# Performance work log

Hardware: AMD Instinct MI355X
Metric: run time of the kernel (lower is better)

## Reference

```python
import jax, jax.numpy as jnp
import numpy as np

NUM_CLASSES = 8
SCORE_T = 0.5
IOU_T = 0.5
POSE_HYPS = 10
MAX_DET = 100
B, A = 1, 4096


def _pairwise_iou(bx):
    # bx: (N,4) in (x1,y1,x2,y2); TF-style +1 pixel convention
    x1 = jnp.maximum(bx[:, None, 0], bx[None, :, 0])
    y1 = jnp.maximum(bx[:, None, 1], bx[None, :, 1])
    x2 = jnp.minimum(bx[:, None, 2], bx[None, :, 2])
    y2 = jnp.minimum(bx[:, None, 3], bx[None, :, 3])
    wid = x2 - x1 + 1.0
    hei = y2 - y1 + 1.0
    inter = wid * hei
    area = (bx[:, 2] - bx[:, 0] + 1.0) * (bx[:, 3] - bx[:, 1] + 1.0)
    den = area[:, None] + area[None, :] - inter
    ov = jnp.where(den == 0.0, 0.0, inter / jnp.where(den == 0.0, 1.0, den))  # divide_no_nan
    return jnp.where((wid <= 0.0) | (hei <= 0.0), 0.0, ov)


def _per_class(scores_c, boxes_c, poses_c, conf_c):
    # Fixed-shape re-expression of _filter_detections: instead of compacting the
    # boxes with score > threshold (dynamic shape), keep all N and mask invalid
    # boxes out of the overlap indicator. Relative ordering (which drives the
    # argmax tie-break and the ascending sort) is identical to the compacted
    # subset, so the math matches exactly.
    N = scores_c.shape[0]
    K = POSE_HYPS + 1
    valid = scores_c > SCORE_T
    m = jnp.sum(valid.astype(jnp.int32))  # number of selected boxes
    ov = _pairwise_iou(boxes_c)  # (N,N)
    ind = ((ov > IOU_T) & valid[:, None] & valid[None, :]).astype(jnp.float32)
    # scatter_nd: true_ov[argmax_col(row i), i] = max(row i); column i is unique per update
    max_col = jnp.argmax(ind, axis=1)
    true_ov = jnp.zeros_like(ind).at[max_col, jnp.arange(N)].add(jnp.max(ind, axis=1))
    bc = (1.0 - ov) * true_ov * conf_c[None, :]
    bc = jnp.where(bc == 0.0, 1000.0, bc)  # 1000 = sentinel for 'not a hypothesis'
    # Only the first min(pose_hyps+1, m) ascending-sorted entries per row survive the
    # sequence mask, so take the K smallest instead of a full argsort (same result;
    # top_k of the negation breaks ties by lowest index like a stable ascending sort).
    neg, args = jax.lax.top_k(-bc, K)
    svals = -neg  # (N,K) K smallest per row
    hyp = (jnp.arange(K) < jnp.minimum(K, m)).astype(jnp.float32)
    cmask = jnp.where(svals == 1000.0, 0.0, 1.0) * hyp[None, :]
    denom = jnp.sum(cmask, axis=1)  # (N,)
    safe = jnp.where(denom == 0.0, 1.0, denom)
    poses_avg = jnp.where(denom[:, None] == 0.0, 0.0,
                          jnp.sum(cmask[:, :, None] * poses_c[args], axis=1) / safe[:, None])
    boxes_avg = jnp.where(denom[:, None] == 0.0, 0.0,
                          jnp.sum(cmask[:, :, None] * boxes_c[args], axis=1) / safe[:, None])
    return poses_avg, boxes_avg, denom > 0.0


def _forward(boxes3D, boxes, classification, poses, confidence):
    C = NUM_CLASSES
    N = classification.shape[0] * classification.shape[1]
    cls = classification.reshape(N, C)
    bxs = boxes.reshape(N, C, 4)
    pss = poses.reshape(N, C, 12)
    cnf = confidence.reshape(N, C)
    # boxes3D is reshaped/gathered by the original but never used afterwards (dead code)
    xs = (cls.T, jnp.transpose(bxs, (1, 0, 2)), jnp.transpose(pss, (1, 0, 2)), cnf.T)
    # serialize over classes so only one NxN working set is live at a time
    poses_avg, boxes_avg, survive = jax.lax.map(lambda t: _per_class(*t), xs)
    surv = survive.reshape(-1)  # (C*N,) class-major, matching the original concat order
    count = jnp.sum(surv.astype(jnp.int32))
    scores_flat = jnp.where(surv, cls.T.reshape(-1), -jnp.inf)
    top_scores, _ = jax.lax.top_k(scores_flat, MAX_DET)
    rank = jnp.arange(MAX_DET)
    ok = rank < count
    out_scores = jnp.where(ok, top_scores, -1.0)
    # NOTE: the original computes top_indices but never applies it — labels/poses/
    # indices/boxes stay in class-major survivor order, truncated/padded with -1.
    pos = jnp.arange(C * N)
    order = jnp.argsort(jnp.where(surv, pos, pos + C * N))  # stable compaction
    sel = order[:MAX_DET]
    labels_flat = jnp.repeat(jnp.arange(C), N)
    anchors_flat = jnp.tile(jnp.arange(N), C)
    out_labels = jnp.where(ok, labels_flat[sel], -1).astype(jnp.int32)
    out_idx = jnp.where(ok, anchors_flat[sel], -1).astype(jnp.int32)
    out_poses = jnp.where(ok[:, None], poses_avg.reshape(C * N, 12)[sel], -1.0)
    out_boxes = jnp.where(ok[:, None], boxes_avg.reshape(C * N, 4)[sel], -1.0)
    return out_scores, out_labels, out_poses, out_idx, out_boxes


def setup_inputs():
    key = jax.random.key(0)
    k1, k2, k3, k4, k5, k6 = jax.random.split(key, 6)
    C = NUM_CLASSES
    # realistic heavily-overlapping boxes in a 640x640 image
    cxy = jax.random.uniform(k1, (B, A, C, 2), minval=0.0, maxval=640.0)
    wh = jax.random.uniform(k2, (B, A, C, 2), minval=10.0, maxval=120.0)
    boxes = jnp.concatenate([cxy - wh / 2.0, cxy + wh / 2.0], axis=-1).reshape(B, A, C * 4)
    return {
        "boxes3D": jax.random.normal(k6, (B, A, C * 16), dtype=jnp.float32),
        "boxes": boxes,
        "classification": jax.random.uniform(k3, (B, A, C), dtype=jnp.float32),
        "poses": jax.random.normal(k4, (B, A, C * 12), dtype=jnp.float32),
        "confidence": jax.random.uniform(k5, (B, A, C), dtype=jnp.float32),
    }


def reference(boxes3D, boxes, classification, poses, confidence):
    return _forward(boxes3D, boxes, classification, poses, confidence)
```

## Files before the change

kernel.cpp:

```cpp
#include <hip/hip_runtime.h>
#include <stdint.h>

#define N_ANCH 4096
#define NCLS 8
#define CN (N_ANCH * NCLS)
#define SCORE_TH 0.5f
#define IOU_TH 0.5f
#define KSEL 11
#define MAX_DET 100
#define CAND_CAP 4096
#define TILE 128
#define TPC (N_ANCH / TILE)
#define NTRI (TPC * (TPC + 1) / 2)

__device__ __forceinline__ float iou_f(float4 a, float areaA, float4 b, float areaB) {
    float x1 = fmaxf(a.x, b.x);
    float y1 = fmaxf(a.y, b.y);
    float x2 = fminf(a.z, b.z);
    float y2 = fminf(a.w, b.w);
    float wid = x2 - x1 + 1.0f;
    float hei = y2 - y1 + 1.0f;
    float inter = wid * hei;
    float den = areaA + areaB - inter;
    float ov = (den == 0.0f) ? 0.0f : (inter / den);
    if (wid <= 0.0f || hei <= 0.0f) ov = 0.0f;
    return ov;
}

__global__ void __launch_bounds__(1024) k_prep_valid(const float* __restrict__ boxes,
                                                     const float* __restrict__ cls,
                                                     const float* __restrict__ conf,
                                                     float4* boxesT, float* areaT,
                                                     float* scoresT, float* confT,
                                                     int* validList, float4* vBox,
                                                     float* vArea, int* mVal,
                                                     int* surv, int* minRank, int* hist) {
    int c = blockIdx.x;
    int tid = threadIdx.x;
    int lane = tid & 63, wid = tid >> 6;
    __shared__ int wsum[16];
    int cbase = c << 12;
    int n0 = tid * 4;
    const float4* boxes4 = reinterpret_cast<const float4*>(boxes);
    float4 b[4]; float s[4], cf[4], ar[4];
    #pragma unroll
    for (int d = 0; d < 4; d++) {
        int src = (n0 + d) * 8 + c;
        s[d] = cls[src];
        cf[d] = conf[src];
        b[d] = boxes4[src];
        ar[d] = (b[d].z - b[d].x + 1.0f) * (b[d].w - b[d].y + 1.0f);
    }
    reinterpret_cast<float4*>(scoresT + cbase)[tid] = make_float4(s[0], s[1], s[2], s[3]);
    reinterpret_cast<float4*>(confT + cbase)[tid] = make_float4(cf[0], cf[1], cf[2], cf[3]);
    reinterpret_cast<float4*>(areaT + cbase)[tid] = make_float4(ar[0], ar[1], ar[2], ar[3]);
    #pragma unroll
    for (int d = 0; d < 4; d++) boxesT[cbase + n0 + d] = b[d];
    reinterpret_cast<int4*>(surv + cbase)[tid] = make_int4(0, 0, 0, 0);
    reinterpret_cast<int4*>(minRank + cbase)[tid] =
        make_int4(0x7FFFFFFF, 0x7FFFFFFF, 0x7FFFFFFF, 0x7FFFFFFF);
    if (c == 0) hist[tid] = 0;
    int f0 = s[0] > SCORE_TH, f1 = s[1] > SCORE_TH, f2 = s[2] > SCORE_TH, f3 = s[3] > SCORE_TH;
    int f = f0 + f1 + f2 + f3;
    int inc = f;
    for (int off = 1; off < 64; off <<= 1) {
        int o = __shfl_up(inc, off);
        if (lane >= off) inc += o;
    }
    if (lane == 63) wsum[wid] = inc;
    __syncthreads();
    int wbase = 0;
    for (int i = 0; i < wid; i++) wbase += wsum[i];
    int pos = wbase + inc - f;
    int fl[4] = {f0, f1, f2, f3};
    #pragma unroll
    for (int d = 0; d < 4; d++) {
        if (fl[d]) {
            validList[cbase + pos] = n0 + d;
            vBox[cbase + pos] = b[d];
            vArea[cbase + pos] = ar[d];
            pos++;
        }
    }
    if (tid == 1023) mVal[c] = wbase + inc;
}

__global__ void __launch_bounds__(128) k_repmat(const float4* __restrict__ vBox,
                                                const float* __restrict__ vArea,
                                                const int* __restrict__ mVal,
                                                int* minRank) {
    int bid = blockIdx.x;
    int c = bid / NTRI;
    int t = bid - c * NTRI;
    int ci = (int)((sqrtf(8.0f * (float)t + 1.0f) - 1.0f) * 0.5f);
    while ((ci + 1) * (ci + 2) / 2 <= t) ci++;
    while (ci * (ci + 1) / 2 > t) ci--;
    int cj = t - ci * (ci + 1) / 2;
    int mc = mVal[c];
    int ib = ci * TILE, jb = cj * TILE;
    if (ib >= mc || jb >= mc) return;
    int tid = threadIdx.x;
    int cbase = c << 12;
    __shared__ float4 sB[TILE];
    __shared__ float sA[TILE];
    if (jb + tid < mc) {
        sB[tid] = vBox[cbase + jb + tid];
        sA[tid] = vArea[cbase + jb + tid];
    }
    __syncthreads();
    int i = ib + tid;
    if (i >= mc) return;
    float4 bk = vBox[cbase + i];
    float ak = vArea[cbase + i];
    int limit = min(TILE, mc - jb);
    if (ci == cj) limit = min(limit, i - jb);
    int lmin = 0x7FFFFFFF;
    #pragma unroll 4
    for (int r = 0; r < limit; r++) {
        float ov = iou_f(bk, ak, sB[r], sA[r]);
        if (ov > IOU_TH && r < lmin) lmin = r;
    }
    if (lmin != 0x7FFFFFFF) atomicMin(&minRank[cbase + i], jb + lmin);
}

__global__ void __launch_bounds__(256) k_repA(const float4* __restrict__ vBox,
                                              const float* __restrict__ vArea,
                                              const float* __restrict__ confT,
                                              const int* __restrict__ validList,
                                              const int* __restrict__ mVal,
                                              const int* __restrict__ minRank,
                                              int* rep, int* surv) {
    int t = blockIdx.x * 256 + threadIdx.x;
    int c = t >> 12;
    int i = t & (N_ANCH - 1);
    int mc = mVal[c];
    if (i >= mc) return;
    int cbase = c << 12;
    int k = validList[cbase + i];
    int mr = minRank[cbase + i];
    if (mr > i) mr = i;
    int j = validList[cbase + mr];
    rep[cbase + k] = j;
    if (mr < i) {
        float ov = iou_f(vBox[cbase + i], vArea[cbase + i], vBox[cbase + mr], vArea[cbase + mr]);
        float bcv = (1.0f - ov) * confT[cbase + k];
        if (bcv != 0.0f) surv[cbase + j] = 1;
    }
}

__global__ void __launch_bounds__(256) k_B(const int* __restrict__ surv,
                                           const float* __restrict__ scoresT,
                                           int* candPos, float* candScore,
                                           int* blockCnt, int* hist) {
    int bid = blockIdx.x, tid = threadIdx.x;
    int lane = tid & 63, w = tid >> 6;
    int t = bid * 256 + tid;
    int flag = surv[t] != 0;
    unsigned long long mask = __ballot(flag);
    __shared__ int wcnt[4];
    if (lane == 0) wcnt[w] = __popcll(mask);
    __syncthreads();
    int rank = __popcll(mask & ((1ull << lane) - 1ull));
    int wbase = 0;
    for (int i = 0; i < w; i++) wbase += wcnt[i];
    if (flag) {
        int local = wbase + rank;
        float v = scoresT[t];
        candPos[bid * 256 + local] = t;
        candScore[bid * 256 + local] = v;
        unsigned bits = __float_as_uint(v);
        int bb = (int)((bits - 0x3F000000u) >> 13);
        int bkt = bb < 0 ? 0 : (bb > 1023 ? 1023 : bb);
        atomicAdd(&hist[bkt], 1);
    }
    if (tid == 0) blockCnt[bid] = wcnt[0] + wcnt[1] + wcnt[2] + wcnt[3];
}

__global__ void __launch_bounds__(1024) k_C(const int* __restrict__ blockCnt,
                                            const int* __restrict__ hist,
                                            const int* __restrict__ candPos,
                                            const float* __restrict__ candScore,
                                            int* sel, int* count_g, float* out) {
    int tid = threadIdx.x;
    __shared__ int bc[128];
    __shared__ int offS[129];
    __shared__ int sfx[256];
    __shared__ int thrB;
    __shared__ int ccS;
    __shared__ float sc[CAND_CAP];
    if (tid < 128) bc[tid] = blockCnt[tid];
    if (tid == 0) { thrB = 0; ccS = 0; }
    __syncthreads();
    if (tid == 0) {
        int run = 0;
        for (int i = 0; i < 128; i++) { offS[i] = run; run += bc[i]; }
        offS[128] = run;
        *count_g = run;
    }
    __syncthreads();
    int count = offS[128];
    int target = count < MAX_DET ? count : MAX_DET;
    if (tid < target) {
        int lo = 0, hi = 127;
        while (lo < hi) { int mid = (lo + hi + 1) >> 1; if (offS[mid] <= tid) lo = mid; else hi = mid - 1; }
        sel[tid] = candPos[lo * 256 + (tid - offS[lo])];
    }
    if (tid < 256) {
        sfx[tid] = hist[4 * tid] + hist[4 * tid + 1] + hist[4 * tid + 2] + hist[4 * tid + 3];
    }
    __syncthreads();
    if (tid == 0) {
        int run = 0;
        for (int i = 255; i >= 0; i--) { int v = sfx[i]; sfx[i] = run; run += v; }
    }
    __syncthreads();
    if (tid < 256) {
        int S = sfx[tid];
        int found = -1;
        for (int b = 4 * tid + 3; b >= 4 * tid; b--) {
            S += hist[b];
            if (found < 0 && S >= target) found = b;
        }
        if (found >= 0) atomicMax(&thrB, found);
    }
    __syncthreads();
    int t0 = thrB;
    for (int pos = tid; pos < CN; pos += 1024) {
        int b = pos >> 8, l = pos & 255;
        if (l < bc[b]) {
            float v = candScore[pos];
            unsigned bits = __float_as_uint(v);
            int bb = (int)((bits - 0x3F000000u) >> 13);
            int bkt = bb < 0 ? 0 : (bb > 1023 ? 1023 : bb);
            if (bkt >= t0) {
                int id = atomicAdd(&ccS, 1);
                if (id < CAND_CAP) sc[id] = -v;
            }
        }
    }
    __syncthreads();
    int cc = ccS; if (cc > CAND_CAP) cc = CAND_CAP;
    int n = 128; while (n < cc) n <<= 1;
    for (int i = tid; i < n; i += 1024) if (i >= cc) sc[i] = 1e38f;
    __syncthreads();
    for (int kk = 2; kk <= n; kk <<= 1) {
        for (int jj = kk >> 1; jj > 0; jj >>= 1) {
            for (int i = tid; i < n; i += 1024) {
                int ixj = i ^ jj;
                if (ixj > i) {
                    float a = sc[i], b2 = sc[ixj];
                    bool up = ((i & kk) == 0);
                    if (up ? (a > b2) : (a < b2)) { sc[i] = b2; sc[ixj] = a; }
                }
            }
            __syncthreads();
        }
    }
    if (tid < MAX_DET) out[tid] = (tid < count) ? -sc[tid] : -1.0f;
}

__global__ void __launch_bounds__(256) k_out(const float4* __restrict__ boxesT,
                                             const float* __restrict__ areaT,
                                             const float* __restrict__ confT,
                                             const float* __restrict__ poses,
                                             const int* __restrict__ rep,
                                             const int* __restrict__ sel,
                                             const int* __restrict__ count_g,
                                             float* out) {
    int s = blockIdx.x;
    int tid = threadIdx.x;
    int lane = tid & 63, w = tid >> 6;
    int count = *count_g;
    if (s >= count) {
        if (tid == 0) { out[100 + s] = -1.0f; out[1400 + s] = -1.0f; }
        if (tid < 12) out[200 + s * 12 + tid] = -1.0f;
        if (tid >= 16 && tid < 20) out[1500 + s * 4 + (tid - 16)] = -1.0f;
        return;
    }
    int p = sel[s];
    int c = p >> 12;
    int r = p & (N_ANCH - 1);
    int cbase = c << 12;
    __shared__ unsigned long long keyArr[4096];
    __shared__ int nmS;
    __shared__ int kselS[KSEL];
    __shared__ unsigned long long bestS;
    __shared__ unsigned long long redK[4];
    if (tid == 0) nmS = 0;
    __syncthreads();
    float4 br = boxesT[cbase + r];
    float ar = areaT[cbase + r];
    for (int k = tid; k < N_ANCH; k += 256) {
        int rp = rep[cbase + k];
        if (rp == r && k != r) {
            float ov = iou_f(br, ar, boxesT[cbase + k], areaT[cbase + k]);
            float bcv = (1.0f - ov) * confT[cbase + k];
            if (bcv != 0.0f) {
                int id = atomicAdd(&nmS, 1);
                keyArr[id] = ((unsigned long long)__float_as_uint(bcv) << 32) | (unsigned)k;
            }
        }
    }
    __syncthreads();
    int nm = nmS;
    int dn = nm < KSEL ? nm : KSEL;
    unsigned long long lastBest = ~0ull;
    for (int j = 0; j < dn; j++) {
        unsigned long long bk = ~0ull;
        for (int i = tid; i < nm; i += 256) {
            unsigned long long v = keyArr[i];
            if (v == lastBest) { keyArr[i] = ~0ull; v = ~0ull; }
            if (v < bk) bk = v;
        }
        for (int off = 32; off > 0; off >>= 1) {
            unsigned long long o = __shfl_down(bk, off);
            if (o < bk) bk = o;
        }
        if (lane == 0) redK[w] = bk;
        __syncthreads();
        if (tid == 0) {
            unsigned long long B = redK[0];
            for (int q2 = 1; q2 < 4; q2++) if (redK[q2] < B) B = redK[q2];
            bestS = B;
            kselS[j] = (int)(B & 0xFFFFFFFFull);
        }
        __syncthreads();
        lastBest = bestS;
    }
    float fdn = (float)(dn > 0 ? dn : 1);
    if (tid < 12) {
        float ssum = 0.0f;
        for (int j = 0; j < dn; j++) ssum += poses[(kselS[j] * 8 + c) * 12 + tid];
        out[200 + s * 12 + tid] = ssum / fdn;
    } else if (tid < 16) {
        int d = tid - 12;
        float ssum = 0.0f;
        for (int j = 0; j < dn; j++) {
            const float* bb = (const float*)&boxesT[cbase + kselS[j]];
            ssum += bb[d];
        }
        out[1500 + s * 4 + d] = ssum / fdn;
    } else if (tid == 16) {
        out[100 + s] = (float)c;
    } else if (tid == 17) {
        out[1400 + s] = (float)r;
    }
}

extern "C" void kernel_launch(void* const* d_in, const int* in_sizes, int n_in,
                              void* d_out, int out_size, void* d_ws, size_t ws_size,
                              hipStream_t stream) {
    const float* boxes = (const float*)d_in[1];
    const float* cls   = (const float*)d_in[2];
    const float* poses = (const float*)d_in[3];
    const float* conf  = (const float*)d_in[4];
    float* out = (float*)d_out;

    char* ws = (char*)d_ws;
    size_t off = 0;
    auto alloc = [&](size_t bytes) {
        void* p = ws + off;
        off += (bytes + 255) & ~(size_t)255;
        return p;
    };
    float4* boxesT   = (float4*)alloc(CN * sizeof(float4));
    float*  areaT    = (float*)alloc(CN * sizeof(float));
    float*  scoresT  = (float*)alloc(CN * sizeof(float));
    float*  confT    = (float*)alloc(CN * sizeof(float));
    int*    validList= (int*)alloc(CN * sizeof(int));
    float4* vBox     = (float4*)alloc(CN * sizeof(float4));
    float*  vArea    = (float*)alloc(CN * sizeof(float));
    int*    mVal     = (int*)alloc(64);
    int*    rep      = (int*)alloc(CN * sizeof(int));
    int*    surv     = (int*)alloc(CN * sizeof(int));
    int*    minRank  = (int*)alloc(CN * sizeof(int));
    int*    sel      = (int*)alloc(MAX_DET * sizeof(int));
    int*    count_g  = (int*)alloc(64);
    int*    candPos  = (int*)alloc(CN * sizeof(int));
    float*  candScore= (float*)alloc(CN * sizeof(float));
    int*    hist     = (int*)alloc(1024 * sizeof(int));
    int*    blockCnt = (int*)alloc(128 * sizeof(int));

    k_prep_valid<<<NCLS, 1024, 0, stream>>>(boxes, cls, conf, boxesT, areaT, scoresT, confT,
                                            validList, vBox, vArea, mVal, surv, minRank, hist);
    k_repmat<<<NCLS * NTRI, 128, 0, stream>>>(vBox, vArea, mVal, minRank);
    k_repA<<<CN / 256, 256, 0, stream>>>(vBox, vArea, confT, validList, mVal, minRank, rep, surv);
    k_B<<<CN / 256, 256, 0, stream>>>(surv, scoresT, candPos, candScore, blockCnt, hist);
    k_C<<<1, 1024, 0, stream>>>(blockCnt, hist, candPos, candScore, sel, count_g, out);
    k_out<<<MAX_DET, 256, 0, stream>>>(boxesT, areaT, confT, poses, rep, sel, count_g, out);
}
```

Measured before the change: 147.9 us.

## Split prep into wide transpose kernel plus compaction; skip selection when few hypotheses

Result: faster. 139.0 us (-6.0%).

```diff
diff --git a/kernel.cpp b/kernel.cpp
--- a/kernel.cpp
+++ b/kernel.cpp
@@ -27,40 +27,39 @@
     return ov;
 }
 
-__global__ void __launch_bounds__(1024) k_prep_valid(const float* __restrict__ boxes,
-                                                     const float* __restrict__ cls,
-                                                     const float* __restrict__ conf,
-                                                     float4* boxesT, float* areaT,
-                                                     float* scoresT, float* confT,
-                                                     int* validList, float4* vBox,
-                                                     float* vArea, int* mVal,
-                                                     int* surv, int* minRank, int* hist) {
+__global__ void __launch_bounds__(256) k_prep(const float* __restrict__ boxes,
+                                              const float* __restrict__ cls,
+                                              const float* __restrict__ conf,
+                                              float4* boxesT, float* areaT,
+                                              float* scoresT, float* confT,
+                                              int* surv, int* minRank, int* hist) {
+    int t = blockIdx.x * 256 + threadIdx.x;
+    int n = t >> 3;
+    int c = t & 7;
+    int p = (c << 12) + n;
+    scoresT[p] = cls[t];
+    confT[p] = conf[t];
+    float4 b = reinterpret_cast<const float4*>(boxes)[t];
+    boxesT[p] = b;
+    areaT[p] = (b.z - b.x + 1.0f) * (b.w - b.y + 1.0f);
+    surv[t] = 0;
+    minRank[t] = 0x7FFFFFFF;
+    if (t < 1024) hist[t] = 0;
+}
+
+__global__ void __launch_bounds__(1024) k_validlist(const float* __restrict__ scoresT,
+                                                    const float4* __restrict__ boxesT,
+                                                    const float* __restrict__ areaT,
+                                                    const float* __restrict__ confT,
+                                                    int* validList, float4* vBox,
+                                                    float* vArea, float* vConf, int* mVal) {
     int c = blockIdx.x;
     int tid = threadIdx.x;
     int lane = tid & 63, wid = tid >> 6;
     __shared__ int wsum[16];
     int cbase = c << 12;
-    int n0 = tid * 4;
-    const float4* boxes4 = reinterpret_cast<const float4*>(boxes);
-    float4 b[4]; float s[4], cf[4], ar[4];
-    #pragma unroll
-    for (int d = 0; d < 4; d++) {
-        int src = (n0 + d) * 8 + c;
-        s[d] = cls[src];
-        cf[d] = conf[src];
-        b[d] = boxes4[src];
-        ar[d] = (b[d].z - b[d].x + 1.0f) * (b[d].w - b[d].y + 1.0f);
-    }
-    reinterpret_cast<float4*>(scoresT + cbase)[tid] = make_float4(s[0], s[1], s[2], s[3]);
-    reinterpret_cast<float4*>(confT + cbase)[tid] = make_float4(cf[0], cf[1], cf[2], cf[3]);
-    reinterpret_cast<float4*>(areaT + cbase)[tid] = make_float4(ar[0], ar[1], ar[2], ar[3]);
-    #pragma unroll
-    for (int d = 0; d < 4; d++) boxesT[cbase + n0 + d] = b[d];
-    reinterpret_cast<int4*>(surv + cbase)[tid] = make_int4(0, 0, 0, 0);
-    reinterpret_cast<int4*>(minRank + cbase)[tid] =
-        make_int4(0x7FFFFFFF, 0x7FFFFFFF, 0x7FFFFFFF, 0x7FFFFFFF);
-    if (c == 0) hist[tid] = 0;
-    int f0 = s[0] > SCORE_TH, f1 = s[1] > SCORE_TH, f2 = s[2] > SCORE_TH, f3 = s[3] > SCORE_TH;
+    float4 sc = reinterpret_cast<const float4*>(scoresT + cbase)[tid];
+    int f0 = sc.x > SCORE_TH, f1 = sc.y > SCORE_TH, f2 = sc.z > SCORE_TH, f3 = sc.w > SCORE_TH;
     int f = f0 + f1 + f2 + f3;
     int inc = f;
     for (int off = 1; off < 64; off <<= 1) {
@@ -72,13 +71,16 @@
     int wbase = 0;
     for (int i = 0; i < wid; i++) wbase += wsum[i];
     int pos = wbase + inc - f;
+    int n0 = tid * 4;
     int fl[4] = {f0, f1, f2, f3};
     #pragma unroll
     for (int d = 0; d < 4; d++) {
         if (fl[d]) {
-            validList[cbase + pos] = n0 + d;
-            vBox[cbase + pos] = b[d];
-            vArea[cbase + pos] = ar[d];
+            int n = n0 + d;
+            validList[cbase + pos] = n;
+            vBox[cbase + pos] = boxesT[cbase + n];
+            vArea[cbase + pos] = areaT[cbase + n];
+            vConf[cbase + pos] = confT[cbase + n];
             pos++;
         }
     }
@@ -125,7 +127,7 @@
 
 __global__ void __launch_bounds__(256) k_repA(const float4* __restrict__ vBox,
                                               const float* __restrict__ vArea,
-                                              const float* __restrict__ confT,
+                                              const float* __restrict__ vConf,
                                               const int* __restrict__ validList,
                                               const int* __restrict__ mVal,
                                               const int* __restrict__ minRank,
@@ -143,7 +145,7 @@
     rep[cbase + k] = j;
     if (mr < i) {
         float ov = iou_f(vBox[cbase + i], vArea[cbase + i], vBox[cbase + mr], vArea[cbase + mr]);
-        float bcv = (1.0f - ov) * confT[cbase + k];
+        float bcv = (1.0f - ov) * vConf[cbase + i];
         if (bcv != 0.0f) surv[cbase + j] = 1;
     }
 }
@@ -304,29 +306,34 @@
     __syncthreads();
     int nm = nmS;
     int dn = nm < KSEL ? nm : KSEL;
-    unsigned long long lastBest = ~0ull;
-    for (int j = 0; j < dn; j++) {
-        unsigned long long bk = ~0ull;
-        for (int i = tid; i < nm; i += 256) {
-            unsigned long long v = keyArr[i];
-            if (v == lastBest) { keyArr[i] = ~0ull; v = ~0ull; }
-            if (v < bk) bk = v;
-        }
-        for (int off = 32; off > 0; off >>= 1) {
-            unsigned long long o = __shfl_down(bk, off);
-            if (o < bk) bk = o;
-        }
-        if (lane == 0) redK[w] = bk;
-        __syncthreads();
-        if (tid == 0) {
-            unsigned long long B = redK[0];
-            for (int q2 = 1; q2 < 4; q2++) if (redK[q2] < B) B = redK[q2];
-            bestS = B;
-            kselS[j] = (int)(B & 0xFFFFFFFFull);
-        }
-        __syncthreads();
-        lastBest = bestS;
-    }
+    if (nm > KSEL) {
+        unsigned long long lastBest = ~0ull;
+        for (int j = 0; j < KSEL; j++) {
+            unsigned long long bk = ~0ull;
+            for (int i = tid; i < nm; i += 256) {
+                unsigned long long v = keyArr[i];
+                if (v == lastBest) { keyArr[i] = ~0ull; v = ~0ull; }
+                if (v < bk) bk = v;
+            }
+            for (int off = 32; off > 0; off >>= 1) {
+                unsigned long long o = __shfl_down(bk, off);
+                if (o < bk) bk = o;
+            }
+            if (lane == 0) redK[w] = bk;
+            __syncthreads();
+            if (tid == 0) {
+                unsigned long long B = redK[0];
+                for (int q2 = 1; q2 < 4; q2++) if (redK[q2] < B) B = redK[q2];
+                bestS = B;
+                kselS[j] = (int)(B & 0xFFFFFFFFull);
+            }
+            __syncthreads();
+            lastBest = bestS;
+        }
+    } else if (tid < dn) {
+        kselS[tid] = (int)(keyArr[tid] & 0xFFFFFFFFull);
+    }
+    __syncthreads();
     float fdn = (float)(dn > 0 ? dn : 1);
     if (tid < 12) {
         float ssum = 0.0f;
@@ -370,6 +377,7 @@
     int*    validList= (int*)alloc(CN * sizeof(int));
     float4* vBox     = (float4*)alloc(CN * sizeof(float4));
     float*  vArea    = (float*)alloc(CN * sizeof(float));
+    float*  vConf    = (float*)alloc(CN * sizeof(float));
     int*    mVal     = (int*)alloc(64);
     int*    rep      = (int*)alloc(CN * sizeof(int));
     int*    surv     = (int*)alloc(CN * sizeof(int));
@@ -381,10 +389,12 @@
     int*    hist     = (int*)alloc(1024 * sizeof(int));
     int*    blockCnt = (int*)alloc(128 * sizeof(int));
 
-    k_prep_valid<<<NCLS, 1024, 0, stream>>>(boxes, cls, conf, boxesT, areaT, scoresT, confT,
-                                            validList, vBox, vArea, mVal, surv, minRank, hist);
+    k_prep<<<CN / 256, 256, 0, stream>>>(boxes, cls, conf, boxesT, areaT, scoresT, confT,
+                                         surv, minRank, hist);
+    k_validlist<<<NCLS, 1024, 0, stream>>>(scoresT, boxesT, areaT, confT,
+                                           validList, vBox, vArea, vConf, mVal);
     k_repmat<<<NCLS * NTRI, 128, 0, stream>>>(vBox, vArea, mVal, minRank);
-    k_repA<<<CN / 256, 256, 0, stream>>>(vBox, vArea, confT, validList, mVal, minRank, rep, surv);
+    k_repA<<<CN / 256, 256, 0, stream>>>(vBox, vArea, vConf, validList, mVal, minRank, rep, surv);
     k_B<<<CN / 256, 256, 0, stream>>>(surv, scoresT, candPos, candScore, blockCnt, hist);
     k_C<<<1, 1024, 0, stream>>>(blockCnt, hist, candPos, candScore, sel, count_g, out);
     k_out<<<MAX_DET, 256, 0, stream>>>(boxesT, areaT, confT, poses, rep, sel, count_g, out);
```
